# Kernel optimization log

Measured on AMD Instinct MI355X. Metric: run time of the kernel, lower is better.

## Reference

```python
import jax, jax.numpy as jnp
import numpy as np

N = 100000   # nodes
E = 400000   # merged window edges
L = 100000   # label edges to decode
DIN = 128
H = 128
NL = 2       # GCN layers
RATIO = 0.8
DOUT = 1


def setup_inputs() -> dict:
    key = jax.random.key(0)
    ks = jax.random.split(key, 24)
    def nrm(k, shape, fan):
        return (jax.random.normal(k, shape, jnp.float32) / np.sqrt(fan)).astype(jnp.float32)
    inp = {
        'x': jax.random.normal(ks[0], (N, DIN), jnp.float32),
        'edge_index': jax.random.randint(ks[1], (2, E), 0, N, jnp.int64) if jax.config.jax_enable_x64 else jax.random.randint(ks[1], (2, E), 0, N, jnp.int32),
        'edge_label_index': jax.random.randint(ks[2], (2, L), 0, N, jnp.int32),
        'edge_time': jax.random.uniform(ks[3], (E,), jnp.float32),
        'previous_state': jax.random.normal(ks[4], (N, H), jnp.float32),
        # mlp_transform: Linear(DIN,H)+ReLU
        'w_mlp': nrm(ks[5], (DIN, H), DIN), 'b_mlp': jnp.zeros((H,), jnp.float32),
        # TimeEncode: cos(Linear(1,H)(t))
        'w_time': nrm(ks[6], (H,), 1), 'b_time': jnp.zeros((H,), jnp.float32),
        # Sampling MLP: Linear(3H,H)+ReLU, Linear(H,1)
        'w_s1': nrm(ks[7], (3 * H, H), 3 * H), 'b_s1': jnp.zeros((H,), jnp.float32),
        'w_s2': nrm(ks[8], (H, 1), H), 'b_s2': jnp.zeros((1,), jnp.float32),
        # GCNConv weights per layer
        'gcn_w': nrm(ks[9], (NL, H, H), H), 'gcn_b': jnp.zeros((NL, H), jnp.float32),
        # GRUCell (stored as [H,3H] so x @ W is the torch x @ W_ih^T)
        'gru_wi': nrm(ks[10], (H, 3 * H), H), 'gru_wh': nrm(ks[11], (H, 3 * H), H),
        'gru_bi': jnp.zeros((3 * H,), jnp.float32), 'gru_bh': jnp.zeros((3 * H,), jnp.float32),
        # LinkDecoder: (h_src * h_dst) @ W + b
        'w_dec': nrm(ks[12], (H, DOUT), H), 'b_dec': jnp.zeros((DOUT,), jnp.float32),
    }
    return inp


def _gcn_pass(h, s2, d2, norm, W, b):
    m = h @ W                                      # [N,H]
    agg = jax.ops.segment_sum(norm[:, None] * m[s2], d2, num_segments=N)
    return agg + b


def reference(x, edge_index, edge_label_index, edge_time, previous_state,
              w_mlp, b_mlp, w_time, b_time, w_s1, b_s1, w_s2, b_s2,
              gcn_w, gcn_b, gru_wi, gru_wh, gru_bi, gru_bh, w_dec, b_dec):
    h = jax.nn.relu(x @ w_mlp + b_mlp)             # [N,H]
    src, dst = edge_index[0], edge_index[1]
    # time encoding of shifted edge times: cos(t*w + b) -> [E,H]
    t = edge_time - edge_time.min() + 1.0
    te = jnp.cos(t[:, None] * w_time + b_time)
    # Sampling logits; concat(prev[src],prev[dst],te) @ w_s1 done as 3 matmuls
    pre = (previous_state[src] @ w_s1[:H] + previous_state[dst] @ w_s1[H:2 * H]
           + te @ w_s1[2 * H:] + b_s1)
    logits = jax.nn.relu(pre) @ w_s2 + b_s2        # [E,1]
    z = jax.nn.sigmoid(logits[:, 0])               # eval mode: no Gumbel noise
    k = int(RATIO * E)
    _, keep = jax.lax.top_k(z, k)
    ew, s, d = z[keep], src[keep], dst[keep]
    # GCN normalization with self-loops (weight 1), symmetric norm as in PyG
    sl = jnp.arange(N, dtype=s.dtype)
    s2 = jnp.concatenate([s, sl]); d2 = jnp.concatenate([d, sl])
    w2 = jnp.concatenate([ew, jnp.ones((N,), ew.dtype)])
    deg = jax.ops.segment_sum(w2, d2, num_segments=N)
    dinv = jnp.where(deg > 0, jax.lax.rsqrt(deg), 0.0)
    norm = dinv[s2] * w2 * dinv[d2]                # [k+N]
    for i in range(NL):
        h = _gcn_pass(h, s2, d2, norm, gcn_w[i], gcn_b[i])
        if i != NL - 1:
            h = jax.nn.relu(h)
    # GRUCell update (torch semantics)
    gi = h @ gru_wi + gru_bi
    gh = previous_state @ gru_wh + gru_bh
    ir, iz, inn = jnp.split(gi, 3, axis=1)
    hr, hz, hn = jnp.split(gh, 3, axis=1)
    r = jax.nn.sigmoid(ir + hr)
    u = jax.nn.sigmoid(iz + hz)
    n = jnp.tanh(inn + r * hn)
    h_new = (1.0 - u) * n + u * previous_state     # [N,H]
    # LinkDecoder: Hadamard of endpoints -> linear
    pred = (h_new[edge_label_index[0]] * h_new[edge_label_index[1]]) @ w_dec + b_dec
    return pred, h_new
```

## Files before the change

kernel.cpp:

```cpp
#include <hip/hip_runtime.h>
#include <hip/hip_bf16.h>
#include <math.h>

typedef __bf16 bf16_t;
typedef bf16_t bf16x8 __attribute__((ext_vector_type(8)));
typedef bf16_t bf16x2 __attribute__((ext_vector_type(2)));
typedef float  f32x4  __attribute__((ext_vector_type(4)));
typedef float  f32x2  __attribute__((ext_vector_type(2)));

__device__ __forceinline__ int clampi(int v, int n) {
    return v < 0 ? 0 : (v > n - 1 ? n - 1 : v);
}

template<int NC>
__global__ __launch_bounds__(256) void gemm128(const bf16_t* __restrict__ A,
        const bf16_t* __restrict__ BT, const float* __restrict__ bias,
        float* __restrict__ Cf, bf16_t* __restrict__ Cb, int M, int dorelu)
{
    constexpr int NT = NC / 16;
    int wave = threadIdx.x >> 6, lane = threadIdx.x & 63;
    int mbase = (blockIdx.x * 4 + wave) * 16;
    if (mbase >= M) return;
    int r = lane & 15, q = lane >> 4;
    int arow = mbase + r; if (arow > M - 1) arow = M - 1;
    f32x4 acc[NT];
#pragma unroll
    for (int t = 0; t < NT; ++t) acc[t] = f32x4{0.f, 0.f, 0.f, 0.f};
    const bf16_t* aptr = A + (size_t)arow * 128 + q * 8;
#pragma unroll
    for (int kk = 0; kk < 4; ++kk) {
        bf16x8 af = *(const bf16x8*)(aptr + kk * 32);
#pragma unroll
        for (int t = 0; t < NT; ++t) {
            bf16x8 bfg = *(const bf16x8*)(BT + (size_t)(t * 16 + r) * 128 + kk * 32 + q * 8);
            acc[t] = __builtin_amdgcn_mfma_f32_16x16x32_bf16(af, bfg, acc[t], 0, 0, 0);
        }
    }
#pragma unroll
    for (int t = 0; t < NT; ++t) {
#pragma unroll
        for (int i = 0; i < 4; ++i) {
            int row = mbase + q * 4 + i;
            if (row < M) {
                int col = t * 16 + r;
                float v = acc[t][i];
                if (bias) v += bias[col];
                if (dorelu) v = fmaxf(v, 0.f);
                if (Cf) Cf[(size_t)row * NC + col] = v;
                if (Cb) Cb[(size_t)row * NC + col] = (bf16_t)v;
            }
        }
    }
}

__global__ __launch_bounds__(256) void gru_k(const bf16_t* __restrict__ xb,
        const float* __restrict__ prevf, const bf16_t* __restrict__ wiT,
        const bf16_t* __restrict__ whT, const float* __restrict__ bi,
        const float* __restrict__ bh, float* __restrict__ hnew, int M)
{
    int wave = threadIdx.x >> 6, lane = threadIdx.x & 63;
    int mbase = (blockIdx.x * 4 + wave) * 16;
    if (mbase >= M) return;
    int r = lane & 15, q = lane >> 4;
    int arow = mbase + r; if (arow > M - 1) arow = M - 1;
    bf16x8 ax[4], ap[4];
#pragma unroll
    for (int kk = 0; kk < 4; ++kk) {
        ax[kk] = *(const bf16x8*)(xb + (size_t)arow * 128 + kk * 32 + q * 8);
        f32x4 p0 = *(const f32x4*)(prevf + (size_t)arow * 128 + kk * 32 + q * 8);
        f32x4 p1 = *(const f32x4*)(prevf + (size_t)arow * 128 + kk * 32 + q * 8 + 4);
        bf16x8 t;
#pragma unroll
        for (int j = 0; j < 4; ++j) { t[j] = (bf16_t)p0[j]; t[j + 4] = (bf16_t)p1[j]; }
        ap[kk] = t;
    }
#pragma unroll
    for (int t3 = 0; t3 < 8; ++t3) {
        f32x4 gi0{0.f,0.f,0.f,0.f}, gi1{0.f,0.f,0.f,0.f}, gi2{0.f,0.f,0.f,0.f};
        f32x4 gh0{0.f,0.f,0.f,0.f}, gh1{0.f,0.f,0.f,0.f}, gh2{0.f,0.f,0.f,0.f};
#pragma unroll
        for (int kk = 0; kk < 4; ++kk) {
            const bf16_t* wi = wiT + (size_t)(t3 * 16 + r) * 128 + kk * 32 + q * 8;
            const bf16_t* wh = whT + (size_t)(t3 * 16 + r) * 128 + kk * 32 + q * 8;
            gi0 = __builtin_amdgcn_mfma_f32_16x16x32_bf16(ax[kk], *(const bf16x8*)wi, gi0, 0, 0, 0);
            gi1 = __builtin_amdgcn_mfma_f32_16x16x32_bf16(ax[kk], *(const bf16x8*)(wi + 128 * 128), gi1, 0, 0, 0);
            gi2 = __builtin_amdgcn_mfma_f32_16x16x32_bf16(ax[kk], *(const bf16x8*)(wi + 256 * 128), gi2, 0, 0, 0);
            gh0 = __builtin_amdgcn_mfma_f32_16x16x32_bf16(ap[kk], *(const bf16x8*)wh, gh0, 0, 0, 0);
            gh1 = __builtin_amdgcn_mfma_f32_16x16x32_bf16(ap[kk], *(const bf16x8*)(wh + 128 * 128), gh1, 0, 0, 0);
            gh2 = __builtin_amdgcn_mfma_f32_16x16x32_bf16(ap[kk], *(const bf16x8*)(wh + 256 * 128), gh2, 0, 0, 0);
        }
        int f = t3 * 16 + r;
        float bif0 = bi[f], bif1 = bi[128 + f], bif2 = bi[256 + f];
        float bhf0 = bh[f], bhf1 = bh[128 + f], bhf2 = bh[256 + f];
#pragma unroll
        for (int i = 0; i < 4; ++i) {
            int row = mbase + q * 4 + i;
            if (row < M) {
                float ir = gi0[i] + bif0, hr = gh0[i] + bhf0;
                float iz = gi1[i] + bif1, hz = gh1[i] + bhf1;
                float inn = gi2[i] + bif2, hn = gh2[i] + bhf2;
                float rg = 1.f / (1.f + expf(-(ir + hr)));
                float ug = 1.f / (1.f + expf(-(iz + hz)));
                float nn = tanhf(inn + rg * hn);
                float hp = prevf[(size_t)row * 128 + f];
                hnew[(size_t)row * 128 + f] = (1.f - ug) * nn + ug * hp;
            }
        }
    }
}

__global__ void transp_k(const float* __restrict__ src, bf16_t* __restrict__ dst,
                         int cols, int ld, int rowoff)
{
    int i = blockIdx.x * blockDim.x + threadIdx.x;
    if (i >= cols * 128) return;
    int n = i >> 7, kk = i & 127;
    dst[i] = (bf16_t)src[(size_t)(rowoff + kk) * ld + n];
}

__global__ void cvtb_k(const float* __restrict__ src, size_t off0,
                       bf16_t* __restrict__ dst, int n)
{
    for (int i = blockIdx.x * blockDim.x + threadIdx.x; i < n; i += gridDim.x * blockDim.x)
        dst[i] = (bf16_t)src[off0 + (size_t)i];
}

__global__ void initall(unsigned* meta, unsigned* bmeta, unsigned* hist1,
                        unsigned* hist2, unsigned* cnt, float* deg, int N, int k)
{
    int i = blockIdx.x * blockDim.x + threadIdx.x;
    int stride = gridDim.x * blockDim.x;
    if (i == 0) { meta[0] = 0x7f800000u; meta[1] = (unsigned)k; meta[8] = 0u; }
    if (i < 64) bmeta[i] = 0u;
    for (int j = i; j < 65536; j += stride) { hist1[j] = 0u; hist2[j] = 0u; }
    for (int j = i; j < N + 1; j += stride) cnt[j] = 0u;
    for (int j = i; j < N; j += stride) deg[j] = 1.0f;
}

__global__ void tmin_k(const float* __restrict__ et, unsigned* meta, int E)
{
    __shared__ float sred[4];
    int i = blockIdx.x * blockDim.x + threadIdx.x;
    int stride = gridDim.x * blockDim.x;
    float v = 1e30f;
    for (; i < E; i += stride) v = fminf(v, et[i]);
    for (int off = 32; off; off >>= 1) v = fminf(v, __shfl_down(v, off, 64));
    int wave = threadIdx.x >> 6, lane = threadIdx.x & 63;
    if (lane == 0) sred[wave] = v;
    __syncthreads();
    if (threadIdx.x == 0) {
        v = fminf(fminf(sred[0], sred[1]), fminf(sred[2], sred[3]));
        atomicMin(meta + 0, __float_as_uint(v));
    }
}

__global__ void bcount_k(const int* __restrict__ ei, unsigned* bmeta, int E, int Nh, int N)
{
    __shared__ unsigned sc[4];
    int tid = threadIdx.x;
    if (tid < 4) sc[tid] = 0;
    __syncthreads();
    int e = blockIdx.x * blockDim.x + tid;
    int b = -1;
    if (e < E) {
        int s = clampi(ei[e], N), d = clampi(ei[E + e], N);
        b = (s >= Nh ? 2 : 0) + (d >= Nh ? 1 : 0);
    }
    int lane = tid & 63;
#pragma unroll
    for (int bb = 0; bb < 4; ++bb) {
        unsigned long long m = __ballot(b == bb);
        if (lane == 0 && m) atomicAdd(sc + bb, (unsigned)__popcll(m));
    }
    __syncthreads();
    if (tid < 4 && sc[tid]) atomicAdd(bmeta + tid, sc[tid]);
}

__global__ void bscan_k(unsigned* bmeta)
{
    if (threadIdx.x == 0 && blockIdx.x == 0) {
        bmeta[4] = 0;
        for (int b = 0; b < 4; ++b) {
            bmeta[5 + b] = bmeta[4 + b] + bmeta[b];
            bmeta[9 + b] = bmeta[4 + b];
        }
    }
}

__global__ void bfill_k(const int* __restrict__ ei, unsigned* bmeta,
                        unsigned* __restrict__ elist, int E, int Nh, int N)
{
    __shared__ unsigned scount[4];
    __shared__ unsigned sbase[4];
    int tid = threadIdx.x;
    if (tid < 4) scount[tid] = 0;
    __syncthreads();
    int e = blockIdx.x * blockDim.x + tid;
    int b = -1;
    if (e < E) {
        int s = clampi(ei[e], N), d = clampi(ei[E + e], N);
        b = (s >= Nh ? 2 : 0) + (d >= Nh ? 1 : 0);
    }
    int lane = tid & 63;
    unsigned myofs = 0;
#pragma unroll
    for (int bb = 0; bb < 4; ++bb) {
        unsigned long long m = __ballot(b == bb);
        unsigned wb = 0;
        if (lane == 0 && m) wb = atomicAdd(scount + bb, (unsigned)__popcll(m));
        wb = __shfl(wb, 0, 64);
        if (b == bb) myofs = wb + (unsigned)__popcll(m & ((1ull << lane) - 1ull));
    }
    __syncthreads();
    if (tid < 4) sbase[tid] = scount[tid] ? atomicAdd(bmeta + 9 + tid, scount[tid]) : 0u;
    __syncthreads();
    if (b >= 0) elist[sbase[b] + myofs] = (unsigned)e;
}

__global__ __launch_bounds__(256, 4) void proj2w16(const float* __restrict__ prevf,
        const float* __restrict__ Wflat, float* __restrict__ out, int rows, int base)
{
    __shared__ float sP[4][16][20];
    int wave = threadIdx.x >> 6, lane = threadIdx.x & 63;
    int rbase = blockIdx.x * 64 + wave * 16;
    if (rbase >= rows) return;
    int tx = lane & 15, eg = lane >> 4;
    int kk = tx, e0 = eg * 4;
    float acc[4][8];
#pragma unroll
    for (int i = 0; i < 4; ++i)
#pragma unroll
        for (int j = 0; j < 8; ++j) acc[i][j] = 0.f;
    for (int kc = 0; kc < 128; kc += 16) {
        float tmp[4];
#pragma unroll
        for (int i = 0; i < 4; ++i) {
            int rr = rbase + e0 + i; if (rr > rows - 1) rr = rows - 1;
            tmp[i] = prevf[(size_t)(base + rr) * 128 + kc + kk];
        }
#pragma unroll
        for (int i = 0; i < 4; ++i) sP[wave][kk][e0 + i] = tmp[i];
        asm volatile("" ::: "memory");
#pragma unroll
        for (int r = 0; r < 16; ++r) {
            f32x4 a0 = *(const f32x4*)&sP[wave][r][e0];
            f32x4 b0 = *(const f32x4*)&Wflat[(size_t)(kc + r) * 128 + tx * 4];
            f32x4 b1 = *(const f32x4*)&Wflat[(size_t)(kc + r) * 128 + 64 + tx * 4];
#pragma unroll
            for (int i = 0; i < 4; ++i) {
#pragma unroll
                for (int j = 0; j < 4; ++j) {
                    acc[i][j]     = fmaf(a0[i], b0[j], acc[i][j]);
                    acc[i][j + 4] = fmaf(a0[i], b1[j], acc[i][j + 4]);
                }
            }
        }
        asm volatile("" ::: "memory");
    }
#pragma unroll
    for (int i = 0; i < 4; ++i) {
        int row = rbase + e0 + i;
        if (row < rows) {
            f32x4 o0, o1;
#pragma unroll
            for (int j = 0; j < 4; ++j) { o0[j] = acc[i][j]; o1[j] = acc[i][j + 4]; }
            *(f32x4*)&out[(size_t)row * 128 + tx * 4] = o0;
            *(f32x4*)&out[(size_t)row * 128 + 64 + tx * 4] = o1;
        }
    }
}

__global__ __launch_bounds__(256, 4) void zgemmw16(
        const float* __restrict__ et, const int* __restrict__ ei,
        const float* __restrict__ Ah, const float* __restrict__ Bh,
        const float* __restrict__ wtime, const float* __restrict__ btime,
        const float* __restrict__ wc, const float* __restrict__ bs1,
        const float* __restrict__ ws2, const float* __restrict__ bs2,
        const unsigned* __restrict__ meta,
        float* __restrict__ z, unsigned* __restrict__ hist1, int E, int N)
{
    int wave = threadIdx.x >> 6, lane = threadIdx.x & 63;
    int base = blockIdx.x * 64 + wave * 16;
    if (base >= E) return;
    __shared__ float sT[4][16];
    __shared__ int sS[4][16], sD[4][16];
    __shared__ float sC[4][16][20];
    if (lane < 16) {
        float tmin = __uint_as_float(meta[0]);
        int slot = base + lane; if (slot > E - 1) slot = E - 1;
        sT[wave][lane] = et[slot] - tmin + 1.0f;
        sS[wave][lane] = clampi(ei[slot], N);
        sD[wave][lane] = clampi(ei[E + slot], N);
    }
    asm volatile("" ::: "memory");
    int tx = lane & 15, eg = lane >> 4;
    int kk = tx, e0 = eg * 4;
    float tv[4];
#pragma unroll
    for (int i = 0; i < 4; ++i) tv[i] = sT[wave][e0 + i];
    float acc[4][8];
#pragma unroll
    for (int i = 0; i < 4; ++i)
#pragma unroll
        for (int j = 0; j < 8; ++j) acc[i][j] = 0.f;
    for (int kc = 0; kc < 128; kc += 16) {
        float wt = wtime[kc + kk], bt = btime[kc + kk];
        float cv[4];
#pragma unroll
        for (int i = 0; i < 4; ++i) cv[i] = cosf(tv[i] * wt + bt);
#pragma unroll
        for (int i = 0; i < 4; ++i) sC[wave][kk][e0 + i] = cv[i];
        asm volatile("" ::: "memory");
#pragma unroll
        for (int r = 0; r < 16; ++r) {
            f32x4 a0 = *(const f32x4*)&sC[wave][r][e0];
            f32x4 b0 = *(const f32x4*)&wc[(size_t)(kc + r) * 128 + tx * 4];
            f32x4 b1 = *(const f32x4*)&wc[(size_t)(kc + r) * 128 + 64 + tx * 4];
#pragma unroll
            for (int i = 0; i < 4; ++i) {
#pragma unroll
                for (int j = 0; j < 4; ++j) {
                    acc[i][j]     = fmaf(a0[i], b0[j], acc[i][j]);
                    acc[i][j + 4] = fmaf(a0[i], b1[j], acc[i][j + 4]);
                }
            }
        }
        asm volatile("" ::: "memory");
    }
    f32x4 bb0 = *(const f32x4*)&bs1[tx * 4];
    f32x4 bb1 = *(const f32x4*)&bs1[64 + tx * 4];
    f32x4 w20 = *(const f32x4*)&ws2[tx * 4];
    f32x4 w21 = *(const f32x4*)&ws2[64 + tx * 4];
    float myv = 0.f;
#pragma unroll
    for (int i = 0; i < 4; ++i) {
        int r = e0 + i;
        int s = sS[wave][r], d = sD[wave][r];
        const float* As = Ah + (size_t)s * 128;
        const float* Bd = Bh + (size_t)d * 128;
        f32x4 A0 = *(const f32x4*)&As[tx * 4];
        f32x4 A1 = *(const f32x4*)&As[64 + tx * 4];
        f32x4 B0 = *(const f32x4*)&Bd[tx * 4];
        f32x4 B1 = *(const f32x4*)&Bd[64 + tx * 4];
        float v[4];
#pragma unroll
        for (int j = 0; j < 4; ++j) {
            float p0 = acc[i][j] + ((A0[j] + B0[j]) + bb0[j]);
            float p1 = acc[i][j + 4] + ((A1[j] + B1[j]) + bb1[j]);
            v[j] = fmaxf(p0, 0.f) * w20[j] + fmaxf(p1, 0.f) * w21[j];
        }
#pragma unroll
        for (int j = 0; j < 4; ++j) {
            v[j] += __shfl_xor(v[j], 8, 64);
            v[j] += __shfl_xor(v[j], 4, 64);
            v[j] += __shfl_xor(v[j], 2, 64);
            v[j] += __shfl_xor(v[j], 1, 64);
        }
        float vv = (v[0] + v[2]) + (v[1] + v[3]);
        if (tx == i) myv = vv;
    }
    if (tx < 4) {
        int slot = base + e0 + tx;
        if (slot < E) {
            float b2 = bs2[0];
            float zv = 1.f / (1.f + expf(-(myv + b2)));
            z[slot] = zv;
            atomicAdd(hist1 + (__float_as_uint(zv) >> 16), 1u);
        }
    }
}

__global__ __launch_bounds__(256, 2) void proj2w(const float* __restrict__ prevf,
        const float* __restrict__ Wflat, float* __restrict__ out, int rows, int base)
{
    __shared__ float sP[4][16][36];
    int wave = threadIdx.x >> 6, lane = threadIdx.x & 63;
    int rbase = blockIdx.x * 128 + wave * 32;
    if (rbase >= rows) return;
    int tx = lane & 15, eg = lane >> 4;
    int kk = lane & 15, e0 = (lane >> 4) * 8;
    float acc[8][8];
#pragma unroll
    for (int i = 0; i < 8; ++i)
#pragma unroll
        for (int j = 0; j < 8; ++j) acc[i][j] = 0.f;
    for (int kc = 0; kc < 128; kc += 16) {
        float tmp[8];
#pragma unroll
        for (int i = 0; i < 8; ++i) {
            int rr = rbase + e0 + i; if (rr > rows - 1) rr = rows - 1;
            tmp[i] = prevf[(size_t)(base + rr) * 128 + kc + kk];
        }
#pragma unroll
        for (int i = 0; i < 8; ++i) sP[wave][kk][e0 + i] = tmp[i];
        asm volatile("" ::: "memory");
#pragma unroll
        for (int r = 0; r < 16; ++r) {
            f32x4 a0 = *(const f32x4*)&sP[wave][r][eg * 8];
            f32x4 a1 = *(const f32x4*)&sP[wave][r][eg * 8 + 4];
            f32x4 b0 = *(const f32x4*)&Wflat[(size_t)(kc + r) * 128 + tx * 4];
            f32x4 b1 = *(const f32x4*)&Wflat[(size_t)(kc + r) * 128 + 64 + tx * 4];
#pragma unroll
            for (int i = 0; i < 8; ++i) {
                float ae = i < 4 ? a0[i] : a1[i - 4];
#pragma unroll
                for (int j = 0; j < 4; ++j) {
                    acc[i][j]     = fmaf(ae, b0[j], acc[i][j]);
                    acc[i][j + 4] = fmaf(ae, b1[j], acc[i][j + 4]);
                }
            }
        }
        asm volatile("" ::: "memory");
    }
#pragma unroll
    for (int i = 0; i < 8; ++i) {
        int row = rbase + eg * 8 + i;
        if (row < rows) {
            f32x4 o0, o1;
#pragma unroll
            for (int j = 0; j < 4; ++j) { o0[j] = acc[i][j]; o1[j] = acc[i][j + 4]; }
            *(f32x4*)&out[(size_t)row * 128 + tx * 4] = o0;
            *(f32x4*)&out[(size_t)row * 128 + 64 + tx * 4] = o1;
        }
    }
}

__global__ __launch_bounds__(256, 2) void zgemmw(
        const float* __restrict__ et, const int* __restrict__ ei,
        const unsigned* __restrict__ elist, const unsigned* __restrict__ bmeta, int b,
        int soff, int doff,
        const float* __restrict__ Ah, const float* __restrict__ Bh,
        const float* __restrict__ wtime, const float* __restrict__ btime,
        const float* __restrict__ wc, const float* __restrict__ bs1,
        const float* __restrict__ ws2, const float* __restrict__ bs2,
        const unsigned* __restrict__ meta,
        float* __restrict__ z, unsigned* __restrict__ hist1, int E, int N)
{
    unsigned lo = 0, hi = (unsigned)E;
    if (b >= 0) { lo = bmeta[4 + b]; hi = bmeta[5 + b]; }
    int wave = threadIdx.x >> 6, lane = threadIdx.x & 63;
    unsigned ebase = (unsigned)blockIdx.x * 128u + (unsigned)wave * 32u;
    if (ebase >= hi - lo) return;
    __shared__ float sT[4][32];
    __shared__ int sS[4][32], sD[4][32];
    __shared__ unsigned sE[4][32];
    __shared__ float sC[4][16][36];
    if (lane < 32) {
        float tmin = __uint_as_float(meta[0]);
        unsigned slot = lo + ebase + (unsigned)lane;
        unsigned sl = slot < hi ? slot : hi - 1u;
        unsigned e = elist ? elist[sl] : sl;
        sE[wave][lane] = e;
        sT[wave][lane] = et[e] - tmin + 1.0f;
        sS[wave][lane] = clampi(ei[e], N) - soff;
        sD[wave][lane] = clampi(ei[E + e], N) - doff;
    }
    asm volatile("" ::: "memory");
    int tx = lane & 15, eg = lane >> 4;
    int kk = lane & 15, e0 = (lane >> 4) * 8;
    float tv[8];
#pragma unroll
    for (int i = 0; i < 8; ++i) tv[i] = sT[wave][e0 + i];
    float acc[8][8];
#pragma unroll
    for (int i = 0; i < 8; ++i)
#pragma unroll
        for (int j = 0; j < 8; ++j) acc[i][j] = 0.f;
    for (int kc = 0; kc < 128; kc += 16) {
        float wt = wtime[kc + kk], bt = btime[kc + kk];
        float cv[8];
#pragma unroll
        for (int i = 0; i < 8; ++i) cv[i] = cosf(tv[i] * wt + bt);
#pragma unroll
        for (int i = 0; i < 8; ++i) sC[wave][kk][e0 + i] = cv[i];
        asm volatile("" ::: "memory");
#pragma unroll
        for (int r = 0; r < 16; ++r) {
            f32x4 a0 = *(const f32x4*)&sC[wave][r][eg * 8];
            f32x4 a1 = *(const f32x4*)&sC[wave][r][eg * 8 + 4];
            f32x4 b0 = *(const f32x4*)&wc[(size_t)(kc + r) * 128 + tx * 4];
            f32x4 b1 = *(const f32x4*)&wc[(size_t)(kc + r) * 128 + 64 + tx * 4];
#pragma unroll
            for (int i = 0; i < 8; ++i) {
                float ae = i < 4 ? a0[i] : a1[i - 4];
#pragma unroll
                for (int j = 0; j < 4; ++j) {
                    acc[i][j]     = fmaf(ae, b0[j], acc[i][j]);
                    acc[i][j + 4] = fmaf(ae, b1[j], acc[i][j + 4]);
                }
            }
        }
        asm volatile("" ::: "memory");
    }
    f32x4 bb0 = *(const f32x4*)&bs1[tx * 4];
    f32x4 bb1 = *(const f32x4*)&bs1[64 + tx * 4];
    f32x4 w20 = *(const f32x4*)&ws2[tx * 4];
    f32x4 w21 = *(const f32x4*)&ws2[64 + tx * 4];
    float myv = 0.f;
#pragma unroll
    for (int i = 0; i < 8; ++i) {
        int r = eg * 8 + i;
        int s = sS[wave][r], d = sD[wave][r];
        const float* As = Ah + (size_t)s * 128;
        const float* Bd = Bh + (size_t)d * 128;
        f32x4 A0 = *(const f32x4*)&As[tx * 4];
        f32x4 A1 = *(const f32x4*)&As[64 + tx * 4];
        f32x4 B0 = *(const f32x4*)&Bd[tx * 4];
        f32x4 B1 = *(const f32x4*)&Bd[64 + tx * 4];
        float v[4];
#pragma unroll
        for (int j = 0; j < 4; ++j) {
            float p0 = acc[i][j] + ((A0[j] + B0[j]) + bb0[j]);
            float p1 = acc[i][j + 4] + ((A1[j] + B1[j]) + bb1[j]);
            v[j] = fmaxf(p0, 0.f) * w20[j] + fmaxf(p1, 0.f) * w21[j];
        }
#pragma unroll
        for (int j = 0; j < 4; ++j) {
            v[j] += __shfl_xor(v[j], 8, 64);
            v[j] += __shfl_xor(v[j], 4, 64);
            v[j] += __shfl_xor(v[j], 2, 64);
            v[j] += __shfl_xor(v[j], 1, 64);
        }
        float vv = (v[0] + v[2]) + (v[1] + v[3]);
        if (tx == i) myv = vv;
    }
    if (tx < 8) {
        int r = eg * 8 + tx;
        unsigned slot = lo + ebase + (unsigned)r;
        if (slot < hi) {
            float b2 = bs2[0];
            float zv = 1.f / (1.f + expf(-(myv + b2)));
            z[sE[wave][r]] = zv;
            atomicAdd(hist1 + (__float_as_uint(zv) >> 16), 1u);
        }
    }
}

__global__ __launch_bounds__(1024) void scank(const unsigned* __restrict__ hist,
                                              unsigned* meta, int kIdx, int outIdx)
{
    __shared__ unsigned s[1024];
    int t = threadIdx.x;
    unsigned K = meta[kIdx];
    unsigned sum = 0;
    for (int i = 0; i < 64; ++i) sum += hist[t * 64 + i];
    s[t] = sum;
    __syncthreads();
    for (int off = 1; off < 1024; off <<= 1) {
        unsigned add = (t + off < 1024) ? s[t + off] : 0u;
        __syncthreads();
        s[t] += add;
        __syncthreads();
    }
    unsigned mine = s[t];
    unsigned after = (t < 1023) ? s[t + 1] : 0u;
    if (mine >= K && after < K) {
        unsigned cum = after;
        for (int b = 63; b >= 0; --b) {
            unsigned c = hist[t * 64 + b];
            cum += c;
            if (cum >= K) {
                meta[outIdx] = (unsigned)(t * 64 + b);
                meta[outIdx + 1] = cum - c;
                meta[outIdx + 2] = K - (cum - c);
                break;
            }
        }
    }
}

__global__ void pass2(const float* __restrict__ z, const unsigned* __restrict__ meta,
                      unsigned* hist2, int E)
{
    int e = blockIdx.x * blockDim.x + threadIdx.x;
    if (e >= E) return;
    unsigned u = __float_as_uint(z[e]);
    if ((u >> 16) == meta[2]) atomicAdd(hist2 + (u & 0xffffu), 1u);
}

__global__ void pass3(const float* __restrict__ z, unsigned* meta,
                      unsigned char* keep, unsigned* eql, int E)
{
    int e = blockIdx.x * blockDim.x + threadIdx.x;
    if (e >= E) return;
    unsigned u = __float_as_uint(z[e]);
    unsigned T = (meta[2] << 16) | (meta[5] & 0xffffu);
    keep[e] = (u > T) ? 1 : 0;
    if (u == T) {
        unsigned slot = atomicAdd(meta + 8, 1u);
        if (slot < 4096u) eql[slot] = (unsigned)e;
    }
}

__global__ void eqres(const unsigned* __restrict__ meta, const unsigned* __restrict__ eql,
                      unsigned char* keep)
{
    __shared__ unsigned list[4096];
    unsigned c = meta[8]; if (c > 4096u) c = 4096u;
    unsigned need = meta[7];
    for (unsigned i = threadIdx.x; i < c; i += blockDim.x) list[i] = eql[i];
    __syncthreads();
    for (unsigned i = threadIdx.x; i < c; i += blockDim.x) {
        unsigned rank = 0;
        for (unsigned j = 0; j < c; ++j) rank += (list[j] < list[i]) ? 1u : 0u;
        if (rank < need) keep[list[i]] = 1;
    }
}

__global__ void degsc(const int* __restrict__ ei, const float* __restrict__ z,
                      const unsigned char* __restrict__ keep, float* deg, int E, int N)
{
    int e = blockIdx.x * blockDim.x + threadIdx.x;
    if (e >= E) return;
    if (keep[e]) atomicAdd(deg + clampi(ei[E + e], N), z[e]);
}

__global__ void dinv_k(float* deg, float* selfn, int N)
{
    int i = blockIdx.x * blockDim.x + threadIdx.x;
    if (i >= N) return;
    float d = deg[i];
    float di = 1.0f / sqrtf(d);
    deg[i] = di;
    selfn[i] = di * di;
}

__global__ void normcnt(const int* __restrict__ ei, const float* __restrict__ z,
                        const unsigned char* __restrict__ keep, const float* __restrict__ dinv,
                        float* normv, unsigned* cnt, int E, int N)
{
    int e = blockIdx.x * blockDim.x + threadIdx.x;
    if (e >= E) return;
    if (keep[e]) {
        int s = clampi(ei[e], N), d = clampi(ei[E + e], N);
        normv[e] = dinv[s] * z[e] * dinv[d];
        atomicAdd(cnt + d, 1u);
    } else {
        normv[e] = 0.f;
    }
}

__global__ __launch_bounds__(1024) void scan_n(unsigned* cnt, unsigned* fill, int N)
{
    __shared__ unsigned s[1024];
    int t = threadIdx.x;
    int per = (N + 1023) >> 10;
    int lo = t * per; if (lo > N) lo = N;
    int hi = lo + per; if (hi > N) hi = N;
    unsigned sum = 0;
    for (int i = lo; i < hi; ++i) sum += cnt[i];
    s[t] = sum;
    __syncthreads();
    for (int off = 1; off < 1024; off <<= 1) {
        unsigned add = (t >= off) ? s[t - off] : 0u;
        __syncthreads();
        s[t] += add;
        __syncthreads();
    }
    unsigned run = (t > 0) ? s[t - 1] : 0u;
    for (int i = lo; i < hi; ++i) {
        unsigned c = cnt[i];
        cnt[i] = run; fill[i] = run;
        run += c;
    }
    if (t == 1023) cnt[N] = run;
}

__global__ void fillk(const int* __restrict__ ei, const unsigned char* __restrict__ keep,
                      unsigned* fill, unsigned* csr, int E, int N)
{
    int e = blockIdx.x * blockDim.x + threadIdx.x;
    if (e >= E) return;
    if (keep[e]) {
        unsigned p = atomicAdd(fill + clampi(ei[E + e], N), 1u);
        csr[p] = (unsigned)e;
    }
}

__global__ __launch_bounds__(256) void agg_k(const bf16_t* __restrict__ m,
        const int* __restrict__ ei, const float* __restrict__ normv,
        const unsigned* __restrict__ ofs, const unsigned* __restrict__ csr,
        const float* __restrict__ selfn, const float* __restrict__ bias,
        float* __restrict__ hout, bf16_t* __restrict__ houtb, int N, int E, int dorelu)
{
    int wave = threadIdx.x >> 6, lane = threadIdx.x & 63;
    int n = blockIdx.x * 4 + wave;
    if (n >= N) return;
    int f = 2 * lane;
    float sn = selfn[n];
    bf16x2 mv = *(const bf16x2*)(m + (size_t)n * 128 + f);
    float a0 = bias[f] + sn * (float)mv[0];
    float a1 = bias[f + 1] + sn * (float)mv[1];
    unsigned lo = ofs[n], hi = ofs[n + 1];
    unsigned deg = hi - lo;
    unsigned cap = deg < 64u ? deg : 64u;
    int s_l = 0; float w_l = 0.f;
    if (lane < (int)cap) {
        unsigned e = csr[lo + lane];
        s_l = clampi(ei[e], N);
        w_l = normv[e];
    }
    for (unsigned j = 0; j < cap; ++j) {
        int s = __shfl(s_l, (int)j, 64);
        float w = __shfl(w_l, (int)j, 64);
        bf16x2 v = *(const bf16x2*)(m + (size_t)s * 128 + f);
        a0 = fmaf(w, (float)v[0], a0);
        a1 = fmaf(w, (float)v[1], a1);
    }
    for (unsigned idx = lo + 64; idx < hi; ++idx) {
        unsigned e = csr[idx];
        int s = clampi(ei[e], N);
        float w = normv[e];
        bf16x2 v = *(const bf16x2*)(m + (size_t)s * 128 + f);
        a0 = fmaf(w, (float)v[0], a0);
        a1 = fmaf(w, (float)v[1], a1);
    }
    if (dorelu) { a0 = fmaxf(a0, 0.f); a1 = fmaxf(a1, 0.f); }
    f32x2 o; o[0] = a0; o[1] = a1;
    *(f32x2*)(hout + (size_t)n * 128 + f) = o;
    if (houtb) {
        bf16x2 ob; ob[0] = (bf16_t)a0; ob[1] = (bf16_t)a1;
        *(bf16x2*)(houtb + (size_t)n * 128 + f) = ob;
    }
}

__global__ __launch_bounds__(256) void decode_k(const int* __restrict__ eli,
        const float* __restrict__ hnew, const float* __restrict__ wdec,
        const float* __restrict__ bdec, float* __restrict__ pred, int L, int N)
{
    int wave = threadIdx.x >> 6, lane = threadIdx.x & 63;
    int l = blockIdx.x * 4 + wave;
    if (l >= L) return;
    int a = clampi(eli[l], N), b = clampi(eli[L + l], N);
    f32x2 ha = *(const f32x2*)(hnew + (size_t)a * 128 + 2 * lane);
    f32x2 hb = *(const f32x2*)(hnew + (size_t)b * 128 + 2 * lane);
    f32x2 w  = *(const f32x2*)(wdec + 2 * lane);
    float acc = ha[0] * hb[0] * w[0] + ha[1] * hb[1] * w[1];
    for (int off = 32; off; off >>= 1) acc += __shfl_down(acc, off, 64);
    if (lane == 0) pred[l] = acc + bdec[0];
}

extern "C" void kernel_launch(void* const* d_in, const int* in_sizes, int n_in,
                              void* d_out, int out_size, void* d_ws, size_t ws_size,
                              hipStream_t stream)
{
    (void)n_in; (void)out_size;
    const float* x      = (const float*)d_in[0];
    const int*   ei     = (const int*)d_in[1];
    const int*   eli    = (const int*)d_in[2];
    const float* etime  = (const float*)d_in[3];
    const float* prev   = (const float*)d_in[4];
    const float* w_mlp  = (const float*)d_in[5];
    const float* b_mlp  = (const float*)d_in[6];
    const float* w_time = (const float*)d_in[7];
    const float* b_time = (const float*)d_in[8];
    const float* w_s1   = (const float*)d_in[9];
    const float* b_s1   = (const float*)d_in[10];
    const float* w_s2   = (const float*)d_in[11];
    const float* b_s2   = (const float*)d_in[12];
    const float* gcn_w  = (const float*)d_in[13];
    const float* gcn_b  = (const float*)d_in[14];
    const float* gru_wi = (const float*)d_in[15];
    const float* gru_wh = (const float*)d_in[16];
    const float* gru_bi = (const float*)d_in[17];
    const float* gru_bh = (const float*)d_in[18];
    const float* w_dec  = (const float*)d_in[19];
    const float* b_dec  = (const float*)d_in[20];

    const int E  = in_sizes[3];
    const int N  = in_sizes[0] / 128;
    const int L  = in_sizes[2] / 2;
    const int K  = (int)(0.8 * (double)E);
    const int Nh = (N + 1) / 2;

    char* wsp = (char*)d_ws;
    size_t off = 0;
    auto alloc = [&](size_t bytes) -> void* {
        void* p = wsp + off;
        off += (bytes + 255) & ~(size_t)255;
        return p;
    };
    unsigned* meta  = (unsigned*)alloc(64 * 4);
    unsigned* bmeta = (unsigned*)alloc(64 * 4);
    unsigned* elist = (unsigned*)alloc((size_t)E * 4);
    unsigned* eql   = (unsigned*)alloc(4096 * 4);
    unsigned* hist1 = (unsigned*)alloc(65536 * 4);
    unsigned* hist2 = (unsigned*)alloc(65536 * 4);
    unsigned* cnt   = (unsigned*)alloc((size_t)(N + 1) * 4);
    unsigned* fill  = (unsigned*)alloc((size_t)N * 4);
    float* deg      = (float*)alloc((size_t)N * 4);
    float* selfn    = (float*)alloc((size_t)N * 4);
    float* zbuf     = (float*)alloc((size_t)E * 4);
    unsigned char* keep = (unsigned char*)alloc((size_t)E);
    float* normv    = (float*)alloc((size_t)E * 4);
    unsigned* csr   = (unsigned*)alloc((size_t)E * 4);
    bf16_t* wmlpT = (bf16_t*)alloc(128 * 128 * 2);
    bf16_t* g0T   = (bf16_t*)alloc(128 * 128 * 2);
    bf16_t* g1T   = (bf16_t*)alloc(128 * 128 * 2);
    bf16_t* wiT   = (bf16_t*)alloc(384 * 128 * 2);
    bf16_t* whT   = (bf16_t*)alloc(384 * 128 * 2);

    size_t fullBytes = (size_t)N * 128 * 4;
    size_t halfBytes = (size_t)Nh * 128 * 4;
    bool full = (off + 2 * ((fullBytes + 255) & ~(size_t)255)) <= ws_size;
    char* slot0; char* slot1;
    float* Ahalf; float* Bhalf;
    if (full) {
        slot0 = (char*)alloc(fullBytes);
        slot1 = (char*)alloc(fullBytes);
        Ahalf = (float*)slot0;
        Bhalf = (float*)slot1;
    } else {
        slot0 = (char*)alloc(halfBytes);
        slot1 = (char*)alloc(halfBytes);
        Ahalf = (float*)slot0;
        Bhalf = (float*)slot1;
    }
    bf16_t* xbf   = (bf16_t*)slot0;
    bf16_t* mbuf  = (bf16_t*)slot1;

    float* out_pred = (float*)d_out;
    float* hnew     = (float*)d_out + L;
    float* hb       = hnew;

    initall<<<1024, 256, 0, stream>>>(meta, bmeta, hist1, hist2, cnt, deg, N, K);

    transp_k<<<64, 256, 0, stream>>>(w_mlp, wmlpT, 128, 128, 0);
    transp_k<<<64, 256, 0, stream>>>(gcn_w, g0T, 128, 128, 0);
    transp_k<<<64, 256, 0, stream>>>(gcn_w, g1T, 128, 128, 128);
    transp_k<<<192, 256, 0, stream>>>(gru_wi, wiT, 384, 384, 0);
    transp_k<<<192, 256, 0, stream>>>(gru_wh, whT, 384, 384, 0);

    tmin_k<<<512, 256, 0, stream>>>(etime, meta, E);

    const float* wc = w_s1 + 256 * 128;
    if (full) {
        proj2w16<<<(N + 63) / 64, 256, 0, stream>>>(prev, w_s1, Ahalf, N, 0);
        proj2w16<<<(N + 63) / 64, 256, 0, stream>>>(prev, w_s1 + 128 * 128, Bhalf, N, 0);
        zgemmw16<<<(E + 63) / 64, 256, 0, stream>>>(etime, ei, Ahalf, Bhalf,
                w_time, b_time, wc, b_s1, w_s2, b_s2, meta, zbuf, hist1, E, N);
    } else {
        const int zgrid = (E + 127) / 128;
        bcount_k<<<(E + 255) / 256, 256, 0, stream>>>(ei, bmeta, E, Nh, N);
        bscan_k<<<1, 64, 0, stream>>>(bmeta);
        bfill_k<<<(E + 255) / 256, 256, 0, stream>>>(ei, bmeta, elist, E, Nh, N);
        const int NA0 = Nh, NA1 = N - Nh;
        auto zlaunch = [&](int b, int so, int doo) {
            zgemmw<<<zgrid, 256, 0, stream>>>(etime, ei, elist, bmeta, b, so, doo,
                    Ahalf, Bhalf, w_time, b_time, wc, b_s1, w_s2, b_s2,
                    meta, zbuf, hist1, E, N);
        };
        proj2w<<<(NA0 + 127) / 128, 256, 0, stream>>>(prev, w_s1, Ahalf, NA0, 0);
        proj2w<<<(NA0 + 127) / 128, 256, 0, stream>>>(prev, w_s1 + 128 * 128, Bhalf, NA0, 0);
        zlaunch(0, 0, 0);
        proj2w<<<(NA1 + 127) / 128, 256, 0, stream>>>(prev, w_s1 + 128 * 128, Bhalf, NA1, Nh);
        zlaunch(1, 0, Nh);
        proj2w<<<(NA1 + 127) / 128, 256, 0, stream>>>(prev, w_s1, Ahalf, NA1, Nh);
        zlaunch(3, Nh, Nh);
        proj2w<<<(NA0 + 127) / 128, 256, 0, stream>>>(prev, w_s1 + 128 * 128, Bhalf, NA0, 0);
        zlaunch(2, Nh, 0);
    }

    scank<<<1, 1024, 0, stream>>>(hist1, meta, 1, 2);
    pass2<<<(E + 255) / 256, 256, 0, stream>>>(zbuf, meta, hist2, E);
    scank<<<1, 1024, 0, stream>>>(hist2, meta, 4, 5);
    pass3<<<(E + 255) / 256, 256, 0, stream>>>(zbuf, meta, keep, eql, E);
    eqres<<<1, 256, 0, stream>>>(meta, eql, keep);

    degsc<<<(E + 255) / 256, 256, 0, stream>>>(ei, zbuf, keep, deg, E, N);
    dinv_k<<<(N + 255) / 256, 256, 0, stream>>>(deg, selfn, N);
    normcnt<<<(E + 255) / 256, 256, 0, stream>>>(ei, zbuf, keep, deg, normv, cnt, E, N);
    scan_n<<<1, 1024, 0, stream>>>(cnt, fill, N);
    fillk<<<(E + 255) / 256, 256, 0, stream>>>(ei, keep, fill, csr, E, N);

    cvtb_k<<<2048, 256, 0, stream>>>(x, 0, xbf, N * 128);
    gemm128<128><<<(N + 63) / 64, 256, 0, stream>>>(xbf, wmlpT, b_mlp, hb, xbf, N, 1);

    gemm128<128><<<(N + 63) / 64, 256, 0, stream>>>(xbf, g0T, nullptr, nullptr, mbuf, N, 0);
    agg_k<<<(N + 3) / 4, 256, 0, stream>>>(mbuf, ei, normv, cnt, csr, selfn, gcn_b, hb, xbf, N, E, 1);
    gemm128<128><<<(N + 63) / 64, 256, 0, stream>>>(xbf, g1T, nullptr, nullptr, mbuf, N, 0);
    agg_k<<<(N + 3) / 4, 256, 0, stream>>>(mbuf, ei, normv, cnt, csr, selfn, gcn_b + 128, hb, xbf, N, E, 0);

    gru_k<<<(N + 63) / 64, 256, 0, stream>>>(xbf, prev, wiT, whT, gru_bi, gru_bh, hnew, N);

    decode_k<<<(L + 3) / 4, 256, 0, stream>>>(eli, hnew, w_dec, b_dec, out_pred, L, N);
}
```

Baseline: 1.679 ms.

## Stage sampling-MLP weights in LDS and enlarge per-thread register tiles

The projection and z-score GEMM kernels used on the full path now copy the 128x128 weight block into shared memory once per block. Each thread also computes an 8x8 output tile instead of 4x8, so a block covers 128 rows instead of 64. This is meant to cut repeated global/L1 weight reads and raise FMA reuse per loaded operand. In exchange it uses about 73KB of LDS per block, more registers, and fewer resident blocks, and every block pays the cost of filling the 64KB weight copy.

```diff
diff --git a/kernel.cpp b/kernel.cpp
--- a/kernel.cpp
+++ b/kernel.cpp
@@ -217,49 +217,56 @@
     if (b >= 0) elist[sbase[b] + myofs] = (unsigned)e;
 }
 
-__global__ __launch_bounds__(256, 4) void proj2w16(const float* __restrict__ prevf,
-        const float* __restrict__ Wflat, float* __restrict__ out, int rows, int base)
-{
-    __shared__ float sP[4][16][20];
-    int wave = threadIdx.x >> 6, lane = threadIdx.x & 63;
-    int rbase = blockIdx.x * 64 + wave * 16;
+__global__ __launch_bounds__(256, 2) void projL(const float* __restrict__ prevf,
+        const float* __restrict__ Wflat, float* __restrict__ out, int rows)
+{
+    __shared__ float sW[128 * 128];
+    __shared__ float sP[4][16][36];
+    int tid = threadIdx.x;
+    for (int i = tid * 4; i < 128 * 128; i += 256 * 4)
+        *(f32x4*)&sW[i] = *(const f32x4*)&Wflat[i];
+    __syncthreads();
+    int wave = tid >> 6, lane = tid & 63;
+    int rbase = blockIdx.x * 128 + wave * 32;
     if (rbase >= rows) return;
     int tx = lane & 15, eg = lane >> 4;
-    int kk = tx, e0 = eg * 4;
-    float acc[4][8];
-#pragma unroll
-    for (int i = 0; i < 4; ++i)
+    int kk = lane & 15, e0 = (lane >> 4) * 8;
+    float acc[8][8];
+#pragma unroll
+    for (int i = 0; i < 8; ++i)
 #pragma unroll
         for (int j = 0; j < 8; ++j) acc[i][j] = 0.f;
     for (int kc = 0; kc < 128; kc += 16) {
-        float tmp[4];
-#pragma unroll
-        for (int i = 0; i < 4; ++i) {
+        float tmp[8];
+#pragma unroll
+        for (int i = 0; i < 8; ++i) {
             int rr = rbase + e0 + i; if (rr > rows - 1) rr = rows - 1;
-            tmp[i] = prevf[(size_t)(base + rr) * 128 + kc + kk];
-        }
-#pragma unroll
-        for (int i = 0; i < 4; ++i) sP[wave][kk][e0 + i] = tmp[i];
+            tmp[i] = prevf[(size_t)rr * 128 + kc + kk];
+        }
+#pragma unroll
+        for (int i = 0; i < 8; ++i) sP[wave][kk][e0 + i] = tmp[i];
         asm volatile("" ::: "memory");
 #pragma unroll
         for (int r = 0; r < 16; ++r) {
-            f32x4 a0 = *(const f32x4*)&sP[wave][r][e0];
-            f32x4 b0 = *(const f32x4*)&Wflat[(size_t)(kc + r) * 128 + tx * 4];
-            f32x4 b1 = *(const f32x4*)&Wflat[(size_t)(kc + r) * 128 + 64 + tx * 4];
-#pragma unroll
-            for (int i = 0; i < 4; ++i) {
+            f32x4 a0 = *(const f32x4*)&sP[wave][r][eg * 8];
+            f32x4 a1 = *(const f32x4*)&sP[wave][r][eg * 8 + 4];
+            f32x4 b0 = *(const f32x4*)&sW[(kc + r) * 128 + tx * 4];
+            f32x4 b1 = *(const f32x4*)&sW[(kc + r) * 128 + 64 + tx * 4];
+#pragma unroll
+            for (int i = 0; i < 8; ++i) {
+                float ae = i < 4 ? a0[i] : a1[i - 4];
 #pragma unroll
                 for (int j = 0; j < 4; ++j) {
-                    acc[i][j]     = fmaf(a0[i], b0[j], acc[i][j]);
-                    acc[i][j + 4] = fmaf(a0[i], b1[j], acc[i][j + 4]);
+                    acc[i][j]     = fmaf(ae, b0[j], acc[i][j]);
+                    acc[i][j + 4] = fmaf(ae, b1[j], acc[i][j + 4]);
                 }
             }
         }
         asm volatile("" ::: "memory");
     }
 #pragma unroll
-    for (int i = 0; i < 4; ++i) {
-        int row = rbase + e0 + i;
+    for (int i = 0; i < 8; ++i) {
+        int row = rbase + eg * 8 + i;
         if (row < rows) {
             f32x4 o0, o1;
 #pragma unroll
@@ -270,7 +277,7 @@
     }
 }
 
-__global__ __launch_bounds__(256, 4) void zgemmw16(
+__global__ __launch_bounds__(256, 2) void zgemmL(
         const float* __restrict__ et, const int* __restrict__ ei,
         const float* __restrict__ Ah, const float* __restrict__ Bh,
         const float* __restrict__ wtime, const float* __restrict__ btime,
@@ -279,49 +286,55 @@
         const unsigned* __restrict__ meta,
         float* __restrict__ z, unsigned* __restrict__ hist1, int E, int N)
 {
-    int wave = threadIdx.x >> 6, lane = threadIdx.x & 63;
-    int base = blockIdx.x * 64 + wave * 16;
-    if (base >= E) return;
-    __shared__ float sT[4][16];
-    __shared__ int sS[4][16], sD[4][16];
-    __shared__ float sC[4][16][20];
-    if (lane < 16) {
+    __shared__ float sW[128 * 128];
+    __shared__ float sT[4][32];
+    __shared__ int sS[4][32], sD[4][32];
+    __shared__ float sC[4][16][36];
+    int tid = threadIdx.x;
+    for (int i = tid * 4; i < 128 * 128; i += 256 * 4)
+        *(f32x4*)&sW[i] = *(const f32x4*)&wc[i];
+    int wave = tid >> 6, lane = tid & 63;
+    int base = blockIdx.x * 128 + wave * 32;
+    if (lane < 32 && base < E) {
         float tmin = __uint_as_float(meta[0]);
         int slot = base + lane; if (slot > E - 1) slot = E - 1;
         sT[wave][lane] = et[slot] - tmin + 1.0f;
         sS[wave][lane] = clampi(ei[slot], N);
         sD[wave][lane] = clampi(ei[E + slot], N);
     }
-    asm volatile("" ::: "memory");
+    __syncthreads();
+    if (base >= E) return;
     int tx = lane & 15, eg = lane >> 4;
-    int kk = tx, e0 = eg * 4;
-    float tv[4];
-#pragma unroll
-    for (int i = 0; i < 4; ++i) tv[i] = sT[wave][e0 + i];
-    float acc[4][8];
-#pragma unroll
-    for (int i = 0; i < 4; ++i)
+    int kk = lane & 15, e0 = (lane >> 4) * 8;
+    float tv[8];
+#pragma unroll
+    for (int i = 0; i < 8; ++i) tv[i] = sT[wave][e0 + i];
+    float acc[8][8];
+#pragma unroll
+    for (int i = 0; i < 8; ++i)
 #pragma unroll
         for (int j = 0; j < 8; ++j) acc[i][j] = 0.f;
     for (int kc = 0; kc < 128; kc += 16) {
         float wt = wtime[kc + kk], bt = btime[kc + kk];
-        float cv[4];
-#pragma unroll
-        for (int i = 0; i < 4; ++i) cv[i] = cosf(tv[i] * wt + bt);
-#pragma unroll
-        for (int i = 0; i < 4; ++i) sC[wave][kk][e0 + i] = cv[i];
+        float cv[8];
+#pragma unroll
+        for (int i = 0; i < 8; ++i) cv[i] = cosf(tv[i] * wt + bt);
+#pragma unroll
+        for (int i = 0; i < 8; ++i) sC[wave][kk][e0 + i] = cv[i];
         asm volatile("" ::: "memory");
 #pragma unroll
         for (int r = 0; r < 16; ++r) {
-            f32x4 a0 = *(const f32x4*)&sC[wave][r][e0];
-            f32x4 b0 = *(const f32x4*)&wc[(size_t)(kc + r) * 128 + tx * 4];
-            f32x4 b1 = *(const f32x4*)&wc[(size_t)(kc + r) * 128 + 64 + tx * 4];
-#pragma unroll
-            for (int i = 0; i < 4; ++i) {
+            f32x4 a0 = *(const f32x4*)&sC[wave][r][eg * 8];
+            f32x4 a1 = *(const f32x4*)&sC[wave][r][eg * 8 + 4];
+            f32x4 b0 = *(const f32x4*)&sW[(kc + r) * 128 + tx * 4];
+            f32x4 b1 = *(const f32x4*)&sW[(kc + r) * 128 + 64 + tx * 4];
+#pragma unroll
+            for (int i = 0; i < 8; ++i) {
+                float ae = i < 4 ? a0[i] : a1[i - 4];
 #pragma unroll
                 for (int j = 0; j < 4; ++j) {
-                    acc[i][j]     = fmaf(a0[i], b0[j], acc[i][j]);
-                    acc[i][j + 4] = fmaf(a0[i], b1[j], acc[i][j + 4]);
+                    acc[i][j]     = fmaf(ae, b0[j], acc[i][j]);
+                    acc[i][j + 4] = fmaf(ae, b1[j], acc[i][j + 4]);
                 }
             }
         }
@@ -333,7 +346,7 @@
     f32x4 w21 = *(const f32x4*)&ws2[64 + tx * 4];
     float myv = 0.f;
 #pragma unroll
-    for (int i = 0; i < 4; ++i) {
+    for (int i = 0; i < 8; ++i) {
         int r = e0 + i;
         int s = sS[wave][r], d = sD[wave][r];
         const float* As = Ah + (size_t)s * 128;
@@ -359,7 +372,7 @@
         float vv = (v[0] + v[2]) + (v[1] + v[3]);
         if (tx == i) myv = vv;
     }
-    if (tx < 4) {
+    if (tx < 8) {
         int slot = base + e0 + tx;
         if (slot < E) {
             float b2 = bs2[0];
@@ -835,9 +848,9 @@
 
     const float* wc = w_s1 + 256 * 128;
     if (full) {
-        proj2w16<<<(N + 63) / 64, 256, 0, stream>>>(prev, w_s1, Ahalf, N, 0);
-        proj2w16<<<(N + 63) / 64, 256, 0, stream>>>(prev, w_s1 + 128 * 128, Bhalf, N, 0);
-        zgemmw16<<<(E + 63) / 64, 256, 0, stream>>>(etime, ei, Ahalf, Bhalf,
+        projL<<<(N + 127) / 128, 256, 0, stream>>>(prev, w_s1, Ahalf, N);
+        projL<<<(N + 127) / 128, 256, 0, stream>>>(prev, w_s1 + 128 * 128, Bhalf, N);
+        zgemmL<<<(E + 127) / 128, 256, 0, stream>>>(etime, ei, Ahalf, Bhalf,
                 w_time, b_time, wc, b_s1, w_s2, b_s2, meta, zbuf, hist1, E, N);
     } else {
         const int zgrid = (E + 127) / 128;
```

Result: faster. 1.536 ms (-8.5%).
